# Kernel tuning notes

Measured on AMD Instinct MI355X. Metric: run time of the kernel, lower is better.

## Reference

```python
import jax, jax.numpy as jnp
import numpy as np

N = 20000        # total atoms (atomic environments)
NFEAT = 2784     # power-spectrum feature size: sum_l n_max[l]^2 * n_pseudo^2
P = 4            # n_pseudo (alchemical pseudo-species)
H = 256          # MLP hidden width
S = 500          # number of structures
NSPEC = 8        # number of chemical species (len(all_species))
AVG_ATOMS = N / S  # average_number_of_atoms used for energy normalization


def setup_inputs() -> dict:
    key = jax.random.key(0)
    ks = jax.random.split(key, 8)
    features = jax.random.normal(ks[0], (N, NFEAT), dtype=jnp.float32)
    species = jax.random.randint(ks[1], (N,), 0, NSPEC)
    structure_idx = jax.random.randint(ks[2], (N,), 0, S)
    # combination matrix: Linear(n_species -> n_pseudo), no bias
    W_comb = jax.random.normal(ks[3], (NSPEC, P), dtype=jnp.float32) / np.float32(np.sqrt(NSPEC))
    # per-pseudo-species MLP weights (bias=False throughout)
    W1 = jax.random.normal(ks[4], (P, NFEAT, H), dtype=jnp.float32) / np.float32(np.sqrt(NFEAT))
    W2 = jax.random.normal(ks[5], (P, H, H), dtype=jnp.float32) / np.float32(np.sqrt(H))
    W3 = jax.random.normal(ks[6], (P, H, H), dtype=jnp.float32) / np.float32(np.sqrt(H))
    W4 = jax.random.normal(ks[7], (P, H, 1), dtype=jnp.float32) / np.float32(np.sqrt(H))
    return {"features": features, "W_comb": W_comb, "W1": W1, "W2": W2,
            "W3": W3, "W4": W4, "species": species, "structure_idx": structure_idx}


def reference(features, W_comb, W1, W2, W3, W4, species, structure_idx):
    # one-hot species encoding followed by combination_matrix linear map.
    # one_hot(species) @ W_comb  ==  W_comb[species]  (gather form, no [N, NSPEC] matmul)
    pseudo_w = W_comb[species]                                   # [N, P]
    # outer-product feature embedding: features[:, :, None] * pseudo_w[:, None, :]
    emb = features[:, :, None] * pseudo_w[:, None, :]            # [N, NFEAT, P]
    # per-pseudo-species MLP (Linear no-bias -> SiLU) x3 -> Linear to scalar,
    # vectorized over the pseudo dimension instead of a Python loop.
    h = jax.nn.silu(jnp.einsum('nfp,pfh->nph', emb, W1))         # [N, P, H]
    h = jax.nn.silu(jnp.einsum('nph,phk->npk', h, W2))           # [N, P, H]
    h = jax.nn.silu(jnp.einsum('nph,phk->npk', h, W3))           # [N, P, H]
    per_pseudo_e = jnp.einsum('nph,pho->npo', h, W4)[..., 0]     # [N, P]
    atomic_energies = per_pseudo_e.sum(axis=1) / np.float32(np.sqrt(P))  # [N]
    # scatter-add atomic energies into per-structure energies (index_add_)
    energies = jax.ops.segment_sum(atomic_energies, structure_idx, num_segments=S)
    return energies / np.float32(AVG_ATOMS)                     # [S]
```

## Files before the change

### kernel.cpp

```cpp
#include <hip/hip_runtime.h>
#include <hip/hip_bf16.h>
#include <stdint.h>

#define N_ATOMS 20000
#define NFEAT   2784
#define KP1     2880
#define KT1     45
#define SS      500
#define NPAD    20224
#define MCOLS   1024

typedef __attribute__((ext_vector_type(8))) short s16x8;
typedef __attribute__((ext_vector_type(4))) float f32x4;

static __device__ __forceinline__ unsigned short f2b(float f) {
    __hip_bfloat16 h = __float2bfloat16(f);
    return __builtin_bit_cast(unsigned short, h);
}
static __device__ __forceinline__ float b2f(unsigned short u) {
    unsigned int x = ((unsigned int)u) << 16;
    return __builtin_bit_cast(float, x);
}

#define GLOAD16(g, l) __builtin_amdgcn_global_load_lds( \
    (const __attribute__((address_space(1))) void*)(g), \
    (__attribute__((address_space(3))) void*)(l), 16, 0, 0)

__global__ void conv_feat(const float* __restrict__ F, unsigned short* __restrict__ out) {
    int row = blockIdx.x;
    int t = threadIdx.x;
    const float4* src = (const float4*)(F + (size_t)row * NFEAT);
    unsigned short* dst = out + (size_t)row * KP1;
    for (int g = t; g < KP1 / 4; g += 256) {
        float4 v;
        if (g < NFEAT / 4) v = src[g];
        else { v.x = 0.f; v.y = 0.f; v.z = 0.f; v.w = 0.f; }
        ushort4 o;
        o.x = f2b(v.x); o.y = f2b(v.y); o.z = f2b(v.z); o.w = f2b(v.w);
        *(ushort4*)(dst + g * 4) = o;
    }
}

__global__ void pack_w(const float* __restrict__ W, unsigned short* __restrict__ Bt,
                       int KD, int KP) {
    __shared__ unsigned short tile[32][256];
    int p = blockIdx.y;
    int f0 = blockIdx.x * 32;
    int t = threadIdx.x;
    #pragma unroll 4
    for (int i = 0; i < 32; ++i) {
        int f = f0 + i;
        float v = (f < KD) ? W[((size_t)p * KD + f) * 256 + t] : 0.f;
        tile[i][t] = f2b(v);
    }
    __syncthreads();
    unsigned short* drow = Bt + (size_t)(p * 256 + t) * KP + f0;
    #pragma unroll
    for (int i = 0; i < 32; i += 4) {
        ushort4 o;
        o.x = tile[i][t]; o.y = tile[i + 1][t]; o.z = tile[i + 2][t]; o.w = tile[i + 3][t];
        *(ushort4*)(drow + i) = o;
    }
}

__global__ void make_pw(const float* __restrict__ Wc, const int* __restrict__ spec,
                        float* __restrict__ pw) {
    int n = blockIdx.x * 256 + threadIdx.x;
    if (n < N_ATOMS) {
        int s = spec[n];
        float4 v = *(const float4*)(Wc + s * 4);
        *(float4*)(pw + n * 4) = v;
    }
}

__global__ void zero_f(float* o, int n) {
    int i = blockIdx.x * 256 + threadIdx.x;
    if (i < n) o[i] = 0.f;
}

__global__ __launch_bounds__(512, 4) void gemm1_pipe(
    const unsigned short* __restrict__ A,
    const unsigned short* __restrict__ Bt,
    const float* __restrict__ pw,
    unsigned short* __restrict__ C)
{
    __shared__ __align__(16) unsigned short lds_a[2 * 8192];
    __shared__ __align__(16) unsigned short lds_b[2 * 8192];

    int bid = blockIdx.x;
    int swz = (bid & 7) * 158 + (bid >> 3);
    int rowTile = swz >> 3;
    int colTile = swz & 7;
    int rowBase = rowTile * 128;
    int colBase = colTile * 128;
    int p = colTile >> 1;

    int t0 = threadIdx.x;
    int wave = t0 >> 6;
    int lane = t0 & 63;
    int wm = wave >> 1;
    int wn = wave & 1;

    int rA = t0 >> 3;
    int ckl = ((t0 & 7) ^ (rA & 7)) << 3;
    const unsigned short* sa = A + (size_t)(rowBase + rA) * KP1 + ckl;
    const unsigned short* sb = Bt + (size_t)(colBase + rA) * KP1 + ckl;

    int ra0 = wm * 32 + (lane & 15);
    int rb0 = wn * 64 + (lane & 15);
    int xr = lane & 7;
    int c0 = lane >> 4;

    f32x4 acc[2][4];
    f32x4 z4 = {0.f, 0.f, 0.f, 0.f};
    #pragma unroll
    for (int i = 0; i < 2; ++i)
        #pragma unroll
        for (int j = 0; j < 4; ++j) acc[i][j] = z4;

#define STAGE1(SB) do { \
    GLOAD16(sa,                     lds_a + (SB) * 8192 + t0 * 8); \
    GLOAD16(sa + (size_t)64 * KP1,  lds_a + (SB) * 8192 + 4096 + t0 * 8); \
    GLOAD16(sb,                     lds_b + (SB) * 8192 + t0 * 8); \
    GLOAD16(sb + (size_t)64 * KP1,  lds_b + (SB) * 8192 + 4096 + t0 * 8); \
    sa += 64; sb += 64; \
} while (0)

    STAGE1(0);
    STAGE1(1);
    asm volatile("s_waitcnt vmcnt(4)" ::: "memory");
    __builtin_amdgcn_s_barrier();
    __builtin_amdgcn_sched_barrier(0);

#define FSTEP(CB) do { \
    s16x8 af[2][2], bv[2][4]; \
    _Pragma("unroll") \
    for (int kk = 0; kk < 2; ++kk) { \
        int ch = ((((kk << 2) | c0) ^ xr) << 3); \
        _Pragma("unroll") \
        for (int fm = 0; fm < 2; ++fm) \
            af[kk][fm] = *(const s16x8*)&lds_a[(CB) * 8192 + (ra0 + fm * 16) * 64 + ch]; \
        _Pragma("unroll") \
        for (int fn = 0; fn < 4; ++fn) \
            bv[kk][fn] = *(const s16x8*)&lds_b[(CB) * 8192 + (rb0 + fn * 16) * 64 + ch]; \
    } \
    asm volatile("s_waitcnt lgkmcnt(0)" ::: "memory"); \
    __builtin_amdgcn_sched_barrier(0); \
    __builtin_amdgcn_s_barrier();             \
    __builtin_amdgcn_sched_barrier(0); \
    STAGE1(CB);                               \
    __builtin_amdgcn_s_setprio(1); \
    _Pragma("unroll") \
    for (int kk = 0; kk < 2; ++kk) \
        _Pragma("unroll") \
        for (int fm = 0; fm < 2; ++fm) \
            _Pragma("unroll") \
            for (int fn = 0; fn < 4; ++fn) \
                acc[fm][fn] = __builtin_amdgcn_mfma_f32_16x16x32_bf16( \
                    af[kk][fm], bv[kk][fn], acc[fm][fn], 0, 0, 0); \
    __builtin_amdgcn_s_setprio(0); \
    asm volatile("s_waitcnt vmcnt(4)" ::: "memory");    \
    __builtin_amdgcn_s_barrier(); \
    __builtin_amdgcn_sched_barrier(0); \
} while (0)

#define TSTEP(CB, DRAIN) do { \
    s16x8 af[2][2], bv[2][4]; \
    _Pragma("unroll") \
    for (int kk = 0; kk < 2; ++kk) { \
        int ch = ((((kk << 2) | c0) ^ xr) << 3); \
        _Pragma("unroll") \
        for (int fm = 0; fm < 2; ++fm) \
            af[kk][fm] = *(const s16x8*)&lds_a[(CB) * 8192 + (ra0 + fm * 16) * 64 + ch]; \
        _Pragma("unroll") \
        for (int fn = 0; fn < 4; ++fn) \
            bv[kk][fn] = *(const s16x8*)&lds_b[(CB) * 8192 + (rb0 + fn * 16) * 64 + ch]; \
    } \
    _Pragma("unroll") \
    for (int kk = 0; kk < 2; ++kk) \
        _Pragma("unroll") \
        for (int fm = 0; fm < 2; ++fm) \
            _Pragma("unroll") \
            for (int fn = 0; fn < 4; ++fn) \
                acc[fm][fn] = __builtin_amdgcn_mfma_f32_16x16x32_bf16( \
                    af[kk][fm], bv[kk][fn], acc[fm][fn], 0, 0, 0); \
    if (DRAIN) { \
        asm volatile("s_waitcnt vmcnt(0)" ::: "memory"); \
        __builtin_amdgcn_s_barrier(); \
        __builtin_amdgcn_sched_barrier(0); \
    } \
} while (0)

    for (int it = 0; it < 21; ++it) {
        FSTEP(0);
        FSTEP(1);
    }
    FSTEP(0);
    TSTEP(1, 1);
    TSTEP(0, 0);
#undef FSTEP
#undef TSTEP
#undef STAGE1

    int rGrp = (lane >> 4) << 2;
    int cLane = lane & 15;
    #pragma unroll
    for (int fm = 0; fm < 2; ++fm) {
        int r0 = rowBase + wm * 32 + fm * 16 + rGrp;
        float pwv[4];
        #pragma unroll
        for (int j = 0; j < 4; ++j) pwv[j] = pw[(size_t)(r0 + j) * 4 + p];
        #pragma unroll
        for (int fn = 0; fn < 4; ++fn) {
            int c = colBase + wn * 64 + fn * 16 + cLane;
            f32x4 a = acc[fm][fn];
            #pragma unroll
            for (int j = 0; j < 4; ++j) {
                float x = a[j] * pwv[j];
                float s = x / (1.f + __expf(-x));
                C[(size_t)(r0 + j) * MCOLS + c] = f2b(s);
            }
        }
    }
}

template<int USE_PW>
__global__ __launch_bounds__(256, 2) void gemm_silu(
    const unsigned short* __restrict__ A, int lda,
    const unsigned short* __restrict__ Bt, int ldb,
    int K, int aOffPerP,
    const float* __restrict__ pw,
    unsigned short* __restrict__ C)
{
    __shared__ __align__(16) unsigned short lds_a[128 * 64];
    __shared__ __align__(16) unsigned short lds_b[128 * 64];

    int bid = blockIdx.x;
    int colTile = bid & 7;
    int rowTile = bid >> 3;
    int rowBase = rowTile * 128;
    int colBase = colTile * 128;
    int p = colBase >> 8;
    int aOff = p * aOffPerP;

    int t = threadIdx.x;
    int wave = t >> 6;
    int lane = t & 63;
    int wm = wave >> 1, wn = wave & 1;

    int trow = t >> 3;
    int kcol = (((t & 7) ^ (trow & 7)) << 3);
    const unsigned short* srcA = A + (size_t)(rowBase + trow) * lda + aOff + kcol;
    const unsigned short* srcB = Bt + (size_t)(colBase + trow) * ldb + kcol;

    f32x4 acc[4][4];
    f32x4 z4 = {0.f, 0.f, 0.f, 0.f};
    #pragma unroll
    for (int i = 0; i < 4; ++i)
        #pragma unroll
        for (int j = 0; j < 4; ++j) acc[i][j] = z4;

    int rb = wm * 64 + (lane & 15);
    int cb = wn * 64 + (lane & 15);
    int c0 = lane >> 4;
    int xr = lane & 7;

    int KT = K >> 6;
    for (int kt = 0; kt < KT; ++kt) {
        #pragma unroll
        for (int i = 0; i < 4; ++i) {
            GLOAD16(srcA + (size_t)i * 32 * lda, lds_a + i * 2048 + wave * 512);
            GLOAD16(srcB + (size_t)i * 32 * ldb, lds_b + i * 2048 + wave * 512);
        }
        srcA += 64; srcB += 64;
        __syncthreads();

        #pragma unroll
        for (int kk = 0; kk < 2; ++kk) {
            s16x8 af[4], bfr[4];
            int ch = (((kk << 2) | c0) ^ xr) << 3;
            #pragma unroll
            for (int fm = 0; fm < 4; ++fm)
                af[fm] = *(const s16x8*)&lds_a[(rb + fm * 16) * 64 + ch];
            #pragma unroll
            for (int fn = 0; fn < 4; ++fn)
                bfr[fn] = *(const s16x8*)&lds_b[(cb + fn * 16) * 64 + ch];
            #pragma unroll
            for (int fm = 0; fm < 4; ++fm)
                #pragma unroll
                for (int fn = 0; fn < 4; ++fn)
                    acc[fm][fn] = __builtin_amdgcn_mfma_f32_16x16x32_bf16(
                        af[fm], bfr[fn], acc[fm][fn], 0, 0, 0);
        }
        __syncthreads();
    }

    int rGrp = (lane >> 4) << 2;
    int cLane = lane & 15;
    #pragma unroll
    for (int fm = 0; fm < 4; ++fm) {
        int r0 = rowBase + wm * 64 + fm * 16 + rGrp;
        float pwv[4];
        if (USE_PW) {
            #pragma unroll
            for (int j = 0; j < 4; ++j) pwv[j] = pw[(size_t)(r0 + j) * 4 + p];
        }
        #pragma unroll
        for (int fn = 0; fn < 4; ++fn) {
            int c = colBase + wn * 64 + fn * 16 + cLane;
            f32x4 a = acc[fm][fn];
            #pragma unroll
            for (int j = 0; j < 4; ++j) {
                float x = a[j];
                if (USE_PW) x *= pwv[j];
                float s = x / (1.f + __expf(-x));
                C[(size_t)(r0 + j) * MCOLS + c] = f2b(s);
            }
        }
    }
}

__global__ void finalize(const unsigned short* __restrict__ h3,
                         const float* __restrict__ W4,
                         const int* __restrict__ sidx,
                         float* __restrict__ out) {
    int atom = blockIdx.x * 4 + (threadIdx.x >> 6);
    int lane = threadIdx.x & 63;
    if (atom >= N_ATOMS) return;
    const uint32_t* hu = (const uint32_t*)(h3 + (size_t)atom * MCOLS) + lane * 8;
    const float* w = W4 + lane * 16;
    float sum = 0.f;
    #pragma unroll
    for (int i = 0; i < 8; ++i) {
        uint32_t u = hu[i];
        sum += b2f((unsigned short)(u & 0xffff)) * w[2 * i];
        sum += b2f((unsigned short)(u >> 16)) * w[2 * i + 1];
    }
    #pragma unroll
    for (int off = 32; off > 0; off >>= 1) sum += __shfl_down(sum, off);
    if (lane == 0) atomicAdd(out + sidx[atom], sum * 0.0125f);
}

extern "C" void kernel_launch(void* const* d_in, const int* in_sizes, int n_in,
                              void* d_out, int out_size, void* d_ws, size_t ws_size,
                              hipStream_t stream) {
    const float* features = (const float*)d_in[0];
    const float* W_comb   = (const float*)d_in[1];
    const float* W1       = (const float*)d_in[2];
    const float* W2       = (const float*)d_in[3];
    const float* W3       = (const float*)d_in[4];
    const float* W4       = (const float*)d_in[5];
    const int*   species  = (const int*)d_in[6];
    const int*   sidx     = (const int*)d_in[7];
    float* out = (float*)d_out;

    char* ws = (char*)d_ws;
    size_t off = 0;
    auto carve = [&](size_t bytes) {
        char* r = ws + off;
        off += (bytes + 255) & ~(size_t)255;
        return r;
    };
    unsigned short* feat = (unsigned short*)carve((size_t)NPAD * KP1 * 2);
    unsigned short* B1t  = (unsigned short*)carve((size_t)1024 * KP1 * 2 + 4096);
    unsigned short* B2t  = (unsigned short*)carve((size_t)1024 * 256 * 2);
    unsigned short* B3t  = (unsigned short*)carve((size_t)1024 * 256 * 2);
    float*          pw   = (float*)carve((size_t)NPAD * 4 * 4);
    unsigned short* h1   = (unsigned short*)carve((size_t)NPAD * 1024 * 2);
    carve(4096);
    unsigned short* h2   = feat;

    conv_feat<<<N_ATOMS, 256, 0, stream>>>(features, feat);
    pack_w<<<dim3(KP1 / 32, 4), 256, 0, stream>>>(W1, B1t, NFEAT, KP1);
    pack_w<<<dim3(8, 4), 256, 0, stream>>>(W2, B2t, 256, 256);
    pack_w<<<dim3(8, 4), 256, 0, stream>>>(W3, B3t, 256, 256);
    make_pw<<<(N_ATOMS + 255) / 256, 256, 0, stream>>>(W_comb, species, pw);
    zero_f<<<2, 256, 0, stream>>>(out, SS);

    gemm1_pipe<<<158 * 8, 512, 0, stream>>>(feat, B1t, pw, h1);
    gemm_silu<0><<<158 * 8, 256, 0, stream>>>(h1, 1024, B2t, 256, 256, 256, nullptr, h2);
    gemm_silu<0><<<158 * 8, 256, 0, stream>>>(h2, 1024, B3t, 256, 256, 256, nullptr, h1);
    finalize<<<N_ATOMS / 4, 256, 0, stream>>>(h1, W4, sidx, out);
}
```

Measured before the change: 315.7 us.

## Fuse fp32-to-bf16 feature conversion into the first GEMM's A-tile loads

Removes the separate conversion kernel that read fp32 features and wrote a padded bf16 copy. The first GEMM now loads fp32 features straight into registers, converts them to bf16 and writes them into swizzled LDS, while B still streams in through direct global-to-LDS loads. Out-of-range rows are clamped to the last atom, and K offsets are clamped to stay inside the feature row. The final all-padding K tile is skipped, saving one pipeline step. The cost is that A traffic inside the GEMM doubles (fp32, re-read by each of the 8 column tiles), and conversion work plus register pressure move into the MFMA loop.

```diff
diff --git a/kernel.cpp b/kernel.cpp
--- a/kernel.cpp
+++ b/kernel.cpp
@@ -5,7 +5,6 @@
 #define N_ATOMS 20000
 #define NFEAT   2784
 #define KP1     2880
-#define KT1     45
 #define SS      500
 #define NPAD    20224
 #define MCOLS   1024
@@ -25,21 +24,6 @@
 #define GLOAD16(g, l) __builtin_amdgcn_global_load_lds( \
     (const __attribute__((address_space(1))) void*)(g), \
     (__attribute__((address_space(3))) void*)(l), 16, 0, 0)
-
-__global__ void conv_feat(const float* __restrict__ F, unsigned short* __restrict__ out) {
-    int row = blockIdx.x;
-    int t = threadIdx.x;
-    const float4* src = (const float4*)(F + (size_t)row * NFEAT);
-    unsigned short* dst = out + (size_t)row * KP1;
-    for (int g = t; g < KP1 / 4; g += 256) {
-        float4 v;
-        if (g < NFEAT / 4) v = src[g];
-        else { v.x = 0.f; v.y = 0.f; v.z = 0.f; v.w = 0.f; }
-        ushort4 o;
-        o.x = f2b(v.x); o.y = f2b(v.y); o.z = f2b(v.z); o.w = f2b(v.w);
-        *(ushort4*)(dst + g * 4) = o;
-    }
-}
 
 __global__ void pack_w(const float* __restrict__ W, unsigned short* __restrict__ Bt,
                        int KD, int KP) {
@@ -78,8 +62,8 @@
     if (i < n) o[i] = 0.f;
 }
 
-__global__ __launch_bounds__(512, 4) void gemm1_pipe(
-    const unsigned short* __restrict__ A,
+__global__ __launch_bounds__(512, 4) void gemm1_fused(
+    const float* __restrict__ F,
     const unsigned short* __restrict__ Bt,
     const float* __restrict__ pw,
     unsigned short* __restrict__ C)
@@ -102,8 +86,17 @@
     int wn = wave & 1;
 
     int rA = t0 >> 3;
-    int ckl = ((t0 & 7) ^ (rA & 7)) << 3;
-    const unsigned short* sa = A + (size_t)(rowBase + rA) * KP1 + ckl;
+    int cl = t0 & 7;
+    int cl8 = cl * 8;
+    int pc = cl ^ (rA & 7);
+    int ar0 = rowBase + rA;      if (ar0 > N_ATOMS - 1) ar0 = N_ATOMS - 1;
+    int ar1 = rowBase + rA + 64; if (ar1 > N_ATOMS - 1) ar1 = N_ATOMS - 1;
+    const float* fa0 = F + (size_t)ar0 * NFEAT;
+    const float* fa1 = F + (size_t)ar1 * NFEAT;
+    unsigned short* wA0 = lds_a + rA * 64 + pc * 8;
+    unsigned short* wA1 = lds_a + (rA + 64) * 64 + pc * 8;
+
+    int ckl = (cl ^ (rA & 7)) << 3;
     const unsigned short* sb = Bt + (size_t)(colBase + rA) * KP1 + ckl;
 
     int ra0 = wm * 32 + (lane & 15);
@@ -118,21 +111,37 @@
         #pragma unroll
         for (int j = 0; j < 4; ++j) acc[i][j] = z4;
 
-#define STAGE1(SB) do { \
-    GLOAD16(sa,                     lds_a + (SB) * 8192 + t0 * 8); \
-    GLOAD16(sa + (size_t)64 * KP1,  lds_a + (SB) * 8192 + 4096 + t0 * 8); \
-    GLOAD16(sb,                     lds_b + (SB) * 8192 + t0 * 8); \
-    GLOAD16(sb + (size_t)64 * KP1,  lds_b + (SB) * 8192 + 4096 + t0 * 8); \
-    sa += 64; sb += 64; \
+#define AWRITE(SB, C0, C1, C2, C3) do { \
+    s16x8 w0, w1; \
+    w0[0] = (short)f2b((C0).x); w0[1] = (short)f2b((C0).y); \
+    w0[2] = (short)f2b((C0).z); w0[3] = (short)f2b((C0).w); \
+    w0[4] = (short)f2b((C1).x); w0[5] = (short)f2b((C1).y); \
+    w0[6] = (short)f2b((C1).z); w0[7] = (short)f2b((C1).w); \
+    w1[0] = (short)f2b((C2).x); w1[1] = (short)f2b((C2).y); \
+    w1[2] = (short)f2b((C2).z); w1[3] = (short)f2b((C2).w); \
+    w1[4] = (short)f2b((C3).x); w1[5] = (short)f2b((C3).y); \
+    w1[6] = (short)f2b((C3).z); w1[7] = (short)f2b((C3).w); \
+    *(s16x8*)(wA0 + (SB) * 8192) = w0; \
+    *(s16x8*)(wA1 + (SB) * 8192) = w1; \
 } while (0)
 
-    STAGE1(0);
-    STAGE1(1);
-    asm volatile("s_waitcnt vmcnt(4)" ::: "memory");
-    __builtin_amdgcn_s_barrier();
-    __builtin_amdgcn_sched_barrier(0);
-
-#define FSTEP(CB) do { \
+#define BGLOAD(SB) do { \
+    GLOAD16(sb, lds_b + (SB) * 8192 + t0 * 8); \
+    GLOAD16(sb + (size_t)64 * KP1, lds_b + (SB) * 8192 + 4096 + t0 * 8); \
+    sb += 64; \
+} while (0)
+
+#define MFMA_ALL \
+    _Pragma("unroll") \
+    for (int kk = 0; kk < 2; ++kk) \
+        _Pragma("unroll") \
+        for (int fm = 0; fm < 2; ++fm) \
+            _Pragma("unroll") \
+            for (int fn = 0; fn < 4; ++fn) \
+                acc[fm][fn] = __builtin_amdgcn_mfma_f32_16x16x32_bf16( \
+                    af[kk][fm], bv[kk][fn], acc[fm][fn], 0, 0, 0)
+
+#define FRAGS(CB) \
     s16x8 af[2][2], bv[2][4]; \
     _Pragma("unroll") \
     for (int kk = 0; kk < 2; ++kk) { \
@@ -143,47 +152,80 @@
         _Pragma("unroll") \
         for (int fn = 0; fn < 4; ++fn) \
             bv[kk][fn] = *(const s16x8*)&lds_b[(CB) * 8192 + (rb0 + fn * 16) * 64 + ch]; \
+    }
+
+    float4 a00, a01, a02, a03;
+    float4 a10, a11, a12, a13;
+    {
+        int ko = cl8;
+        a00 = *(const float4*)(fa0 + ko);
+        a01 = *(const float4*)(fa0 + ko + 4);
+        a02 = *(const float4*)(fa1 + ko);
+        a03 = *(const float4*)(fa1 + ko + 4);
+    }
+    __builtin_amdgcn_sched_barrier(0);
+    {
+        int ko = 64 + cl8;
+        a10 = *(const float4*)(fa0 + ko);
+        a11 = *(const float4*)(fa0 + ko + 4);
+        a12 = *(const float4*)(fa1 + ko);
+        a13 = *(const float4*)(fa1 + ko + 4);
+    }
+    __builtin_amdgcn_sched_barrier(0);
+    asm volatile("s_waitcnt vmcnt(4)" ::: "memory");
+    AWRITE(0, a00, a01, a02, a03);
+    BGLOAD(0);
+    asm volatile("s_waitcnt vmcnt(2)" ::: "memory");
+    AWRITE(1, a10, a11, a12, a13);
+    {
+        int ko = 128 + cl8;
+        a00 = *(const float4*)(fa0 + ko);
+        a01 = *(const float4*)(fa0 + ko + 4);
+        a02 = *(const float4*)(fa1 + ko);
+        a03 = *(const float4*)(fa1 + ko + 4);
+    }
+    __builtin_amdgcn_sched_barrier(0);
+    BGLOAD(1);
+    asm volatile("s_waitcnt vmcnt(6) lgkmcnt(0)" ::: "memory");
+    __builtin_amdgcn_s_barrier();
+    __builtin_amdgcn_sched_barrier(0);
+
+    int aik = 192;
+
+#define FSTEP(CB, C0, C1, C2, C3, L0, L1, L2, L3, DO_AI, WN) do { \
+    FRAGS(CB); \
+    asm volatile("s_waitcnt lgkmcnt(0)" ::: "memory"); \
+    __builtin_amdgcn_sched_barrier(0); \
+    __builtin_amdgcn_s_barrier();             \
+    __builtin_amdgcn_sched_barrier(0); \
+    asm volatile("s_waitcnt vmcnt(2)" ::: "memory");   \
+    __builtin_amdgcn_sched_barrier(0); \
+    AWRITE(CB, C0, C1, C2, C3); \
+    if (DO_AI) { \
+        int ko = aik + cl8; if (ko > NFEAT - 8) ko = NFEAT - 8; \
+        L0 = *(const float4*)(fa0 + ko); \
+        L1 = *(const float4*)(fa0 + ko + 4); \
+        L2 = *(const float4*)(fa1 + ko); \
+        L3 = *(const float4*)(fa1 + ko + 4); \
+        aik += 64; \
     } \
+    __builtin_amdgcn_sched_barrier(0); \
+    BGLOAD(CB); \
+    __builtin_amdgcn_s_setprio(1); \
+    MFMA_ALL; \
+    __builtin_amdgcn_s_setprio(0); \
+    asm volatile("s_waitcnt vmcnt(" #WN ") lgkmcnt(0)" ::: "memory");  \
+    __builtin_amdgcn_s_barrier(); \
+    __builtin_amdgcn_sched_barrier(0); \
+} while (0)
+
+#define TSTEP(CB, DRAIN) do { \
+    FRAGS(CB); \
     asm volatile("s_waitcnt lgkmcnt(0)" ::: "memory"); \
     __builtin_amdgcn_sched_barrier(0); \
-    __builtin_amdgcn_s_barrier();             \
-    __builtin_amdgcn_sched_barrier(0); \
-    STAGE1(CB);                               \
     __builtin_amdgcn_s_setprio(1); \
-    _Pragma("unroll") \
-    for (int kk = 0; kk < 2; ++kk) \
-        _Pragma("unroll") \
-        for (int fm = 0; fm < 2; ++fm) \
-            _Pragma("unroll") \
-            for (int fn = 0; fn < 4; ++fn) \
-                acc[fm][fn] = __builtin_amdgcn_mfma_f32_16x16x32_bf16( \
-                    af[kk][fm], bv[kk][fn], acc[fm][fn], 0, 0, 0); \
+    MFMA_ALL; \
     __builtin_amdgcn_s_setprio(0); \
-    asm volatile("s_waitcnt vmcnt(4)" ::: "memory");    \
-    __builtin_amdgcn_s_barrier(); \
-    __builtin_amdgcn_sched_barrier(0); \
-} while (0)
-
-#define TSTEP(CB, DRAIN) do { \
-    s16x8 af[2][2], bv[2][4]; \
-    _Pragma("unroll") \
-    for (int kk = 0; kk < 2; ++kk) { \
-        int ch = ((((kk << 2) | c0) ^ xr) << 3); \
-        _Pragma("unroll") \
-        for (int fm = 0; fm < 2; ++fm) \
-            af[kk][fm] = *(const s16x8*)&lds_a[(CB) * 8192 + (ra0 + fm * 16) * 64 + ch]; \
-        _Pragma("unroll") \
-        for (int fn = 0; fn < 4; ++fn) \
-            bv[kk][fn] = *(const s16x8*)&lds_b[(CB) * 8192 + (rb0 + fn * 16) * 64 + ch]; \
-    } \
-    _Pragma("unroll") \
-    for (int kk = 0; kk < 2; ++kk) \
-        _Pragma("unroll") \
-        for (int fm = 0; fm < 2; ++fm) \
-            _Pragma("unroll") \
-            for (int fn = 0; fn < 4; ++fn) \
-                acc[fm][fn] = __builtin_amdgcn_mfma_f32_16x16x32_bf16( \
-                    af[kk][fm], bv[kk][fn], acc[fm][fn], 0, 0, 0); \
     if (DRAIN) { \
         asm volatile("s_waitcnt vmcnt(0)" ::: "memory"); \
         __builtin_amdgcn_s_barrier(); \
@@ -191,16 +233,20 @@
     } \
 } while (0)
 
-    for (int it = 0; it < 21; ++it) {
-        FSTEP(0);
-        FSTEP(1);
-    }
-    FSTEP(0);
-    TSTEP(1, 1);
-    TSTEP(0, 0);
+    for (int it = 0; it < 20; ++it) {
+        FSTEP(0, a00, a01, a02, a03, a10, a11, a12, a13, 1, 6);
+        FSTEP(1, a10, a11, a12, a13, a00, a01, a02, a03, 1, 6);
+    }
+    FSTEP(0, a00, a01, a02, a03, a10, a11, a12, a13, 1, 6);
+    FSTEP(1, a10, a11, a12, a13, a00, a01, a02, a03, 0, 2);
+    TSTEP(0, 1);
+    TSTEP(1, 0);
 #undef FSTEP
 #undef TSTEP
-#undef STAGE1
+#undef FRAGS
+#undef MFMA_ALL
+#undef BGLOAD
+#undef AWRITE
 
     int rGrp = (lane >> 4) << 2;
     int cLane = lane & 15;
@@ -361,23 +407,21 @@
         off += (bytes + 255) & ~(size_t)255;
         return r;
     };
-    unsigned short* feat = (unsigned short*)carve((size_t)NPAD * KP1 * 2);
     unsigned short* B1t  = (unsigned short*)carve((size_t)1024 * KP1 * 2 + 4096);
     unsigned short* B2t  = (unsigned short*)carve((size_t)1024 * 256 * 2);
     unsigned short* B3t  = (unsigned short*)carve((size_t)1024 * 256 * 2);
     float*          pw   = (float*)carve((size_t)NPAD * 4 * 4);
     unsigned short* h1   = (unsigned short*)carve((size_t)NPAD * 1024 * 2);
+    unsigned short* h2   = (unsigned short*)carve((size_t)NPAD * 1024 * 2);
     carve(4096);
-    unsigned short* h2   = feat;
-
-    conv_feat<<<N_ATOMS, 256, 0, stream>>>(features, feat);
+
     pack_w<<<dim3(KP1 / 32, 4), 256, 0, stream>>>(W1, B1t, NFEAT, KP1);
     pack_w<<<dim3(8, 4), 256, 0, stream>>>(W2, B2t, 256, 256);
     pack_w<<<dim3(8, 4), 256, 0, stream>>>(W3, B3t, 256, 256);
     make_pw<<<(N_ATOMS + 255) / 256, 256, 0, stream>>>(W_comb, species, pw);
     zero_f<<<2, 256, 0, stream>>>(out, SS);
 
-    gemm1_pipe<<<158 * 8, 512, 0, stream>>>(feat, B1t, pw, h1);
+    gemm1_fused<<<158 * 8, 512, 0, stream>>>(features, B1t, pw, h1);
     gemm_silu<0><<<158 * 8, 256, 0, stream>>>(h1, 1024, B2t, 256, 256, 256, nullptr, h2);
     gemm_silu<0><<<158 * 8, 256, 0, stream>>>(h2, 1024, B3t, 256, 256, 256, nullptr, h1);
     finalize<<<N_ATOMS / 4, 256, 0, stream>>>(h1, W4, sidx, out);
```

Result: slower. 374.1 us (+18.5%).

## Fuse layers two, three and the final projection into one LDS-resident tail kernel

Applied to the files above, without the earlier changes.

Replaces the two separate 256-wide GEMM+SiLU launches and the finalize kernel with a single kernel. Each block loads a 64-row by 256-column slice of h1 for one pseudo-species into swizzled LDS and runs layers 2 and 3 there. B operands are read straight from global memory rather than staged in LDS. The W4 dot product and atomic scatter then run in the same block, which removes the global round trips for h2 and h3 and two kernel launches. The trade-off is more LDS per block (64 KB) and B fragments streamed from L2/global each k-step.

```diff
diff --git a/kernel.cpp b/kernel.cpp
--- a/kernel.cpp
+++ b/kernel.cpp
@@ -224,121 +224,116 @@
     }
 }
 
-template<int USE_PW>
-__global__ __launch_bounds__(256, 2) void gemm_silu(
-    const unsigned short* __restrict__ A, int lda,
-    const unsigned short* __restrict__ Bt, int ldb,
-    int K, int aOffPerP,
-    const float* __restrict__ pw,
-    unsigned short* __restrict__ C)
+__global__ __launch_bounds__(256, 2) void mlp_tail(
+    const unsigned short* __restrict__ h1,
+    const unsigned short* __restrict__ B2t,
+    const unsigned short* __restrict__ B3t,
+    const float* __restrict__ W4,
+    const int* __restrict__ sidx,
+    float* __restrict__ out)
 {
-    __shared__ __align__(16) unsigned short lds_a[128 * 64];
-    __shared__ __align__(16) unsigned short lds_b[128 * 64];
+    __shared__ __align__(16) unsigned short bufA[64 * 256];
+    __shared__ __align__(16) unsigned short bufH[64 * 256];
 
     int bid = blockIdx.x;
-    int colTile = bid & 7;
-    int rowTile = bid >> 3;
-    int rowBase = rowTile * 128;
-    int colBase = colTile * 128;
-    int p = colBase >> 8;
-    int aOff = p * aOffPerP;
+    int p  = bid & 3;
+    int rg = bid >> 2;
+    int r0 = rg * 64;
 
     int t = threadIdx.x;
     int wave = t >> 6;
     int lane = t & 63;
-    int wm = wave >> 1, wn = wave & 1;
-
-    int trow = t >> 3;
-    int kcol = (((t & 7) ^ (trow & 7)) << 3);
-    const unsigned short* srcA = A + (size_t)(rowBase + trow) * lda + aOff + kcol;
-    const unsigned short* srcB = Bt + (size_t)(colBase + trow) * ldb + kcol;
+    int rl = lane & 15;
+    int hi = lane >> 4;
+    int rGrp = hi << 2;
+
+    {
+        int pcs = t & 31;
+        #pragma unroll
+        for (int i = 0; i < 8; ++i) {
+            int row_s = i * 8 + (t >> 5);
+            int lcs = (pcs & 24) | ((pcs & 7) ^ (row_s & 7));
+            const unsigned short* g =
+                h1 + ((size_t)(r0 + row_s) * MCOLS + p * 256 + lcs * 8);
+            GLOAD16(g, bufA + i * 2048 + t * 8);
+        }
+    }
+    __syncthreads();
 
     f32x4 acc[4][4];
     f32x4 z4 = {0.f, 0.f, 0.f, 0.f};
-    #pragma unroll
-    for (int i = 0; i < 4; ++i)
-        #pragma unroll
-        for (int j = 0; j < 4; ++j) acc[i][j] = z4;
-
-    int rb = wm * 64 + (lane & 15);
-    int cb = wn * 64 + (lane & 15);
-    int c0 = lane >> 4;
-    int xr = lane & 7;
-
-    int KT = K >> 6;
-    for (int kt = 0; kt < KT; ++kt) {
-        #pragma unroll
-        for (int i = 0; i < 4; ++i) {
-            GLOAD16(srcA + (size_t)i * 32 * lda, lds_a + i * 2048 + wave * 512);
-            GLOAD16(srcB + (size_t)i * 32 * ldb, lds_b + i * 2048 + wave * 512);
+
+#define LAYER(SRC, BT, DST) do { \
+    _Pragma("unroll") \
+    for (int i = 0; i < 4; ++i) \
+        _Pragma("unroll") \
+        for (int j = 0; j < 4; ++j) acc[i][j] = z4; \
+    const unsigned short* bp = (BT) + ((size_t)(p * 256 + wave * 64 + rl) * 256); \
+    _Pragma("unroll") \
+    for (int ks = 0; ks < 8; ++ks) { \
+        s16x8 af[4], bv[4]; \
+        _Pragma("unroll") \
+        for (int fn = 0; fn < 4; ++fn) \
+            bv[fn] = *(const s16x8*)(bp + (size_t)fn * 16 * 256 + ks * 32 + hi * 8); \
+        _Pragma("unroll") \
+        for (int fm = 0; fm < 4; ++fm) { \
+            int row = fm * 16 + rl; \
+            int lc = ks * 4 + hi; \
+            int pc = (lc & 24) | ((lc & 7) ^ (row & 7)); \
+            af[fm] = *(const s16x8*)&(SRC)[row * 256 + pc * 8]; \
+        } \
+        _Pragma("unroll") \
+        for (int fm = 0; fm < 4; ++fm) \
+            _Pragma("unroll") \
+            for (int fn = 0; fn < 4; ++fn) \
+                acc[fm][fn] = __builtin_amdgcn_mfma_f32_16x16x32_bf16( \
+                    af[fm], bv[fn], acc[fm][fn], 0, 0, 0); \
+    } \
+     \
+     \
+     \
+    _Pragma("unroll") \
+    for (int fm = 0; fm < 4; ++fm) \
+        _Pragma("unroll") \
+        for (int fn = 0; fn < 4; ++fn) { \
+            _Pragma("unroll") \
+            for (int j = 0; j < 4; ++j) { \
+                int row = fm * 16 + rGrp + j; \
+                int col = wave * 64 + fn * 16 + rl; \
+                float x = acc[fm][fn][j]; \
+                float s = x / (1.f + __expf(-x)); \
+                int lc = col >> 3; \
+                int pc = (lc & 24) | ((lc & 7) ^ (row & 7)); \
+                (DST)[row * 256 + pc * 8 + (col & 7)] = f2b(s); \
+            } \
+        } \
+    __syncthreads(); \
+} while (0)
+
+    LAYER(bufA, B2t, bufH);
+    LAYER(bufH, B3t, bufA);
+#undef LAYER
+
+    {
+        int row = t >> 2;
+        int q = t & 3;
+        const float* w4 = W4 + p * 256;
+        float sum = 0.f;
+        #pragma unroll
+        for (int c = 0; c < 8; ++c) {
+            int lc = q * 8 + c;
+            int pc = (lc & 24) | ((lc & 7) ^ (row & 7));
+            s16x8 v = *(const s16x8*)&bufA[row * 256 + pc * 8];
+            #pragma unroll
+            for (int e = 0; e < 8; ++e)
+                sum += b2f((unsigned short)v[e]) * w4[lc * 8 + e];
         }
-        srcA += 64; srcB += 64;
-        __syncthreads();
-
-        #pragma unroll
-        for (int kk = 0; kk < 2; ++kk) {
-            s16x8 af[4], bfr[4];
-            int ch = (((kk << 2) | c0) ^ xr) << 3;
-            #pragma unroll
-            for (int fm = 0; fm < 4; ++fm)
-                af[fm] = *(const s16x8*)&lds_a[(rb + fm * 16) * 64 + ch];
-            #pragma unroll
-            for (int fn = 0; fn < 4; ++fn)
-                bfr[fn] = *(const s16x8*)&lds_b[(cb + fn * 16) * 64 + ch];
-            #pragma unroll
-            for (int fm = 0; fm < 4; ++fm)
-                #pragma unroll
-                for (int fn = 0; fn < 4; ++fn)
-                    acc[fm][fn] = __builtin_amdgcn_mfma_f32_16x16x32_bf16(
-                        af[fm], bfr[fn], acc[fm][fn], 0, 0, 0);
-        }
-        __syncthreads();
-    }
-
-    int rGrp = (lane >> 4) << 2;
-    int cLane = lane & 15;
-    #pragma unroll
-    for (int fm = 0; fm < 4; ++fm) {
-        int r0 = rowBase + wm * 64 + fm * 16 + rGrp;
-        float pwv[4];
-        if (USE_PW) {
-            #pragma unroll
-            for (int j = 0; j < 4; ++j) pwv[j] = pw[(size_t)(r0 + j) * 4 + p];
-        }
-        #pragma unroll
-        for (int fn = 0; fn < 4; ++fn) {
-            int c = colBase + wn * 64 + fn * 16 + cLane;
-            f32x4 a = acc[fm][fn];
-            #pragma unroll
-            for (int j = 0; j < 4; ++j) {
-                float x = a[j];
-                if (USE_PW) x *= pwv[j];
-                float s = x / (1.f + __expf(-x));
-                C[(size_t)(r0 + j) * MCOLS + c] = f2b(s);
-            }
-        }
-    }
-}
-
-__global__ void finalize(const unsigned short* __restrict__ h3,
-                         const float* __restrict__ W4,
-                         const int* __restrict__ sidx,
-                         float* __restrict__ out) {
-    int atom = blockIdx.x * 4 + (threadIdx.x >> 6);
-    int lane = threadIdx.x & 63;
-    if (atom >= N_ATOMS) return;
-    const uint32_t* hu = (const uint32_t*)(h3 + (size_t)atom * MCOLS) + lane * 8;
-    const float* w = W4 + lane * 16;
-    float sum = 0.f;
-    #pragma unroll
-    for (int i = 0; i < 8; ++i) {
-        uint32_t u = hu[i];
-        sum += b2f((unsigned short)(u & 0xffff)) * w[2 * i];
-        sum += b2f((unsigned short)(u >> 16)) * w[2 * i + 1];
-    }
-    #pragma unroll
-    for (int off = 32; off > 0; off >>= 1) sum += __shfl_down(sum, off);
-    if (lane == 0) atomicAdd(out + sidx[atom], sum * 0.0125f);
+        sum += __shfl_down(sum, 2);
+        sum += __shfl_down(sum, 1);
+        int atom = r0 + row;
+        if (q == 0 && atom < N_ATOMS)
+            atomicAdd(out + sidx[atom], sum * 0.0125f);
+    }
 }
 
 extern "C" void kernel_launch(void* const* d_in, const int* in_sizes, int n_in,
@@ -368,7 +363,6 @@
     float*          pw   = (float*)carve((size_t)NPAD * 4 * 4);
     unsigned short* h1   = (unsigned short*)carve((size_t)NPAD * 1024 * 2);
     carve(4096);
-    unsigned short* h2   = feat;
 
     conv_feat<<<N_ATOMS, 256, 0, stream>>>(features, feat);
     pack_w<<<dim3(KP1 / 32, 4), 256, 0, stream>>>(W1, B1t, NFEAT, KP1);
@@ -378,7 +372,5 @@
     zero_f<<<2, 256, 0, stream>>>(out, SS);
 
     gemm1_pipe<<<158 * 8, 512, 0, stream>>>(feat, B1t, pw, h1);
-    gemm_silu<0><<<158 * 8, 256, 0, stream>>>(h1, 1024, B2t, 256, 256, 256, nullptr, h2);
-    gemm_silu<0><<<158 * 8, 256, 0, stream>>>(h2, 1024, B3t, 256, 256, 256, nullptr, h1);
-    finalize<<<N_ATOMS / 4, 256, 0, stream>>>(h1, W4, sidx, out);
-}
+    mlp_tail<<<316 * 4, 256, 0, stream>>>(h1, B2t, B3t, W4, sidx, out);
+}
```

Result: slower. 328.2 us (+4.0%).

## Shrink padded K to 2816 and merge small prep kernels into one launch

Applied to the files above, without the earlier changes.

Reduces the padded feature dimension for the first GEMM from 2880 to 2816 (45 to 44 K-tiles), dropping one K-step of zero-padded MFMA work and trimming the pipeline epilogue to match. It also fuses the W2/W3 packing, the pseudo-weight gather and the output zeroing into a single prep kernel, cutting four launches down to one. The K reduction relies on the conversion and packing kernels zero-padding correctly to the new width, and the reworked tail steps must keep the double-buffer ordering consistent.

```diff
diff --git a/kernel.cpp b/kernel.cpp
--- a/kernel.cpp
+++ b/kernel.cpp
@@ -4,8 +4,8 @@
 
 #define N_ATOMS 20000
 #define NFEAT   2784
-#define KP1     2880
-#define KT1     45
+#define KP1     2816
+#define KT1     44
 #define SS      500
 #define NPAD    20224
 #define MCOLS   1024
@@ -63,19 +63,42 @@
     }
 }
 
-__global__ void make_pw(const float* __restrict__ Wc, const int* __restrict__ spec,
-                        float* __restrict__ pw) {
-    int n = blockIdx.x * 256 + threadIdx.x;
-    if (n < N_ATOMS) {
-        int s = spec[n];
-        float4 v = *(const float4*)(Wc + s * 4);
-        *(float4*)(pw + n * 4) = v;
-    }
-}
-
-__global__ void zero_f(float* o, int n) {
-    int i = blockIdx.x * 256 + threadIdx.x;
-    if (i < n) o[i] = 0.f;
+__global__ void prep_small(const float* __restrict__ W2, const float* __restrict__ W3,
+                           unsigned short* __restrict__ B2t, unsigned short* __restrict__ B3t,
+                           const float* __restrict__ Wc, const int* __restrict__ spec,
+                           float* __restrict__ pw, float* __restrict__ out) {
+    __shared__ unsigned short tile[32][256];
+    int b = blockIdx.x;
+    int t = threadIdx.x;
+    if (b < 64) {
+        const float* W = (b < 32) ? W2 : W3;
+        unsigned short* Bt = (b < 32) ? B2t : B3t;
+        int bb = b & 31;
+        int p = bb >> 3;
+        int f0 = (bb & 7) * 32;
+        #pragma unroll 4
+        for (int i = 0; i < 32; ++i) {
+            int f = f0 + i;
+            tile[i][t] = f2b(W[((size_t)p * 256 + f) * 256 + t]);
+        }
+        __syncthreads();
+        unsigned short* drow = Bt + (size_t)(p * 256 + t) * 256 + f0;
+        #pragma unroll
+        for (int i = 0; i < 32; i += 4) {
+            ushort4 o;
+            o.x = tile[i][t]; o.y = tile[i + 1][t]; o.z = tile[i + 2][t]; o.w = tile[i + 3][t];
+            *(ushort4*)(drow + i) = o;
+        }
+    } else if (b < 143) {
+        int n = (b - 64) * 256 + t;
+        if (n < N_ATOMS) {
+            int s = spec[n];
+            float4 v = *(const float4*)(Wc + s * 4);
+            *(float4*)(pw + n * 4) = v;
+        }
+    } else {
+        for (int i = t; i < SS; i += 256) out[i] = 0.f;
+    }
 }
 
 __global__ __launch_bounds__(512, 4) void gemm1_pipe(
@@ -195,9 +218,8 @@
         FSTEP(0);
         FSTEP(1);
     }
-    FSTEP(0);
-    TSTEP(1, 1);
-    TSTEP(0, 0);
+    TSTEP(0, 1);
+    TSTEP(1, 0);
 #undef FSTEP
 #undef TSTEP
 #undef STAGE1
@@ -372,10 +394,7 @@
 
     conv_feat<<<N_ATOMS, 256, 0, stream>>>(features, feat);
     pack_w<<<dim3(KP1 / 32, 4), 256, 0, stream>>>(W1, B1t, NFEAT, KP1);
-    pack_w<<<dim3(8, 4), 256, 0, stream>>>(W2, B2t, 256, 256);
-    pack_w<<<dim3(8, 4), 256, 0, stream>>>(W3, B3t, 256, 256);
-    make_pw<<<(N_ATOMS + 255) / 256, 256, 0, stream>>>(W_comb, species, pw);
-    zero_f<<<2, 256, 0, stream>>>(out, SS);
+    prep_small<<<144, 256, 0, stream>>>(W2, W3, B2t, B3t, W_comb, species, pw, out);
 
     gemm1_pipe<<<158 * 8, 512, 0, stream>>>(feat, B1t, pw, h1);
     gemm_silu<0><<<158 * 8, 256, 0, stream>>>(h1, 1024, B2t, 256, 256, 256, nullptr, h2);
```

Measured after the change: 284.9 us. 1.11x faster.
